# Kernel tuning notes

Hardware: AMD Instinct MI355X
Metric: run time of the kernel (lower is better)

## Reference

```python
import jax, jax.numpy as jnp
import numpy as np
import math

BS, H, L, D = 4, 8, 1024, 64
P = 513  # max_path_num + 1


def setup_inputs() -> dict:
    key = jax.random.key(0)
    ks = jax.random.split(key, 6)
    return {
        "query": jax.random.normal(ks[0], (BS, H, L, D), dtype=jnp.float32),
        "key": jax.random.normal(ks[1], (BS, H, L, D), dtype=jnp.float32),
        "value": jax.random.normal(ks[2], (BS, H, L, D), dtype=jnp.float32),
        "relation": jax.random.normal(ks[3], (BS, P, D), dtype=jnp.float32),
        "path_map": jax.random.randint(ks[4], (BS, L, L), 0, P, dtype=jnp.int32),
        "mask": jax.random.randint(ks[5], (BS, 1, L, L), 0, 2, dtype=jnp.int32),
    }


def reference(query, key, value, relation, path_map, mask):
    bs, h, Lc, d = query.shape
    p = relation.shape[1]
    # content score: bs,h,L,L
    score = jnp.einsum("bhik,bhjk->bhij", query, key)
    # relation score. Torch gathers with index of shape (bs,1,L,L) from a
    # (bs,h,L,P) tensor, which reads head 0 only and broadcasts over heads.
    score_r_h0 = jnp.einsum("bik,bpk->bip", query[:, 0], relation)  # bs,L,P
    gathered = jnp.take_along_axis(score_r_h0, path_map, axis=-1)   # bs,L,L
    score = score + gathered[:, None, :, :]
    scores = score / math.sqrt(d)
    scores = jnp.where(mask == 0, jnp.float32(-1e9), scores)
    p_attn = jax.nn.softmax(scores, axis=-1)  # bs,h,L,L
    attn_sum = jnp.einsum("bhij,bhjk->bhik", p_attn, value)
    # scatter-add attention probs into relation buckets: bs,h,L,P
    b_ix = jnp.arange(bs)[:, None, None, None]
    h_ix = jnp.arange(h)[None, :, None, None]
    i_ix = jnp.arange(Lc)[None, None, :, None]
    pm = jnp.broadcast_to(path_map[:, None, :, :], (bs, h, Lc, Lc))
    r_buckets = jnp.zeros((bs, h, Lc, p), dtype=p_attn.dtype).at[b_ix, h_ix, i_ix, pm].add(p_attn)
    r_attn_sum = jnp.einsum("bhip,bpk->bhik", r_buckets, relation)
    attn_sum = attn_sum + r_attn_sum
    return (attn_sum, p_attn)
```

## Files before the change

kernel.cpp:

```cpp
#include <hip/hip_runtime.h>


#define BSZ 4
#define NH 8
#define LSEQ 1024
#define DH 64
#define NP 513
#define TI 16
#define SRX 548
#define RTC 544

#define NQE (BSZ*NH*LSEQ*DH)
#define NRT (BSZ*DH*RTC)
#define NSR (BSZ*LSEQ*NP)
#define NGPW (2*BSZ*LSEQ*LSEQ)
#define OFF_QH 0
#define OFF_QL (NQE)
#define OFF_KH (2*NQE)
#define OFF_KL (3*NQE)
#define OFF_VT (4*NQE)
#define OFF_RT (5*NQE)
#define OFF_SR (5*NQE + NRT)
#define OFF_GP (5*NQE + NRT + NSR)
#define WS_NEED ((size_t)(OFF_GP + NGPW) * 2)

#define NB_SR 512
#define NB_QK 4096
#define NB_VT 512
#define NB_RT 544
#define NB_P1 (NB_SR + NB_QK + NB_VT + NB_RT)

typedef __attribute__((ext_vector_type(8))) short bf16x8;
typedef __attribute__((ext_vector_type(4))) float f32x4;
typedef __attribute__((ext_vector_type(4))) ushort u16x4;
typedef __attribute__((ext_vector_type(4))) uint u32x4;

__device__ __forceinline__ ushort f2bf(float x) {
    uint u = __float_as_uint(x);
    u += 0x7FFFu + ((u >> 16) & 1u);
    return (ushort)(u >> 16);
}
__device__ __forceinline__ float bf2f(ushort h) {
    return __uint_as_float(((uint)h) << 16);
}


__global__ __launch_bounds__(256) void prep1(
    const float* __restrict__ Q, const float* __restrict__ K,
    const float* __restrict__ V, const float* __restrict__ REL,
    ushort* __restrict__ ws)
{
    __shared__ float sT[64 * 65];
    const int bid = blockIdx.x;
    const int tid = threadIdx.x;

    if (bid < NB_SR) {
        const int b = bid >> 7;
        const int r = bid & 127;
        const int it = r >> 1, half = r & 1;
        const int i0 = it * TI;
        const int w = tid >> 6, l = tid & 63, lg = l >> 4, lm = l & 15;

        const float* Qb0 = Q + ((size_t)b * NH) * LSEQ * DH;
        const float* RELb = REL + (size_t)b * NP * DH;
        ushort* SRb = ws + OFF_SR + (size_t)b * LSEQ * NP;

        bf16x8 qh[2], ql[2];
        #pragma unroll
        for (int ks = 0; ks < 2; ++ks) {
            const float* qs = Qb0 + (size_t)(i0 + lm) * DH + ks * 32 + lg * 8;
            float4 v0 = *(const float4*)(qs);
            float4 v1 = *(const float4*)(qs + 4);
            float xs[8] = {v0.x, v0.y, v0.z, v0.w, v1.x, v1.y, v1.z, v1.w};
            #pragma unroll
            for (int e = 0; e < 8; ++e) {
                ushort hi = f2bf(xs[e]);
                qh[ks][e] = (short)hi;
                ql[ks][e] = (short)f2bf(xs[e] - bf2f(hi));
            }
        }

        int ctb = half ? 33 : 16;
        for (int ct = half * 16 + w; ct < ctb; ct += 4) {
            int p0 = ct * 16;
            int prow = p0 + lm; if (prow > 512) prow = 512;
            f32x4 a0 = {0.f, 0.f, 0.f, 0.f};
            #pragma unroll
            for (int ks = 0; ks < 2; ++ks) {
                const float* bsrc = RELb + (size_t)prow * DH + ks * 32 + lg * 8;
                float4 v0 = *(const float4*)(bsrc);
                float4 v1 = *(const float4*)(bsrc + 4);
                float xs[8] = {v0.x, v0.y, v0.z, v0.w, v1.x, v1.y, v1.z, v1.w};
                bf16x8 bh8, bl8;
                #pragma unroll
                for (int e = 0; e < 8; ++e) {
                    ushort hi = f2bf(xs[e]);
                    bh8[e] = (short)hi;
                    bl8[e] = (short)f2bf(xs[e] - bf2f(hi));
                }
                a0 = __builtin_amdgcn_mfma_f32_16x16x32_bf16(qh[ks], bh8, a0, 0, 0, 0);
                a0 = __builtin_amdgcn_mfma_f32_16x16x32_bf16(ql[ks], bh8, a0, 0, 0, 0);
                a0 = __builtin_amdgcn_mfma_f32_16x16x32_bf16(qh[ks], bl8, a0, 0, 0, 0);
            }
            if (p0 + lm < NP) {
                #pragma unroll
                for (int e = 0; e < 4; ++e)
                    SRb[(size_t)(i0 + 4 * lg + e) * NP + p0 + lm] = f2bf(a0[e]);
            }
        }
    } else if (bid < NB_SR + NB_QK) {
        const int n4 = NQE / 4;
        int i = (bid - NB_SR) * 256 + tid;
        int isK = i >= n4;
        int base = i - isK * n4;
        float4 v = ((const float4*)(isK ? K : Q))[base];
        float xs[4] = {v.x, v.y, v.z, v.w};
        u16x4 hh, ll;
        #pragma unroll
        for (int e = 0; e < 4; ++e) {
            ushort hi = f2bf(xs[e]);
            hh[e] = hi;
            ll[e] = f2bf(xs[e] - bf2f(hi));
        }
        *(u16x4*)(ws + (isK ? OFF_KH : OFF_QH) + (size_t)base * 4) = hh;
        *(u16x4*)(ws + (isK ? OFF_KL : OFF_QL) + (size_t)base * 4) = ll;
    } else if (bid < NB_SR + NB_QK + NB_VT) {
        const int vb = bid - (NB_SR + NB_QK);
        const int bh = vb >> 4;
        const int j0 = (vb & 15) * 64;
        const float* Vb = V + ((size_t)bh << 16);
        for (int i = tid; i < 1024; i += 256) {
            int jr = i >> 4, c4 = i & 15;
            float4 vv = *(const float4*)(Vb + (size_t)(j0 + jr) * DH + c4 * 4);
            float* dst = &sT[jr * 65 + c4 * 4];
            dst[0] = vv.x; dst[1] = vv.y; dst[2] = vv.z; dst[3] = vv.w;
        }
        __syncthreads();
        const int d = tid >> 2, jseg = tid & 3;
        ushort* dst = ws + OFF_VT + ((size_t)bh << 16) + (size_t)d * LSEQ + j0 + jseg * 16;
        #pragma unroll
        for (int g = 0; g < 4; ++g) {
            u16x4 o;
            #pragma unroll
            for (int e = 0; e < 4; ++e)
                o[e] = f2bf(sT[(jseg * 16 + g * 4 + e) * 65 + d]);
            *(u16x4*)(dst + g * 4) = o;
        }
    } else {
        int i = (bid - (NB_SR + NB_QK + NB_VT)) * 256 + tid;
        int b = i / (DH * RTC);
        int r = i - b * (DH * RTC);
        int d = r / RTC;
        int p = r - d * RTC;
        float x = (p < NP) ? REL[((size_t)b * NP + p) * DH + d] : 0.f;
        ws[OFF_RT + i] = f2bf(x);
    }
}


__global__ __launch_bounds__(256) void prep2(
    const int* __restrict__ PM, const int* __restrict__ MASK,
    ushort* __restrict__ ws)
{
    __shared__ ushort sSR[4 * 520];
    const int tid = threadIdx.x;
    const int bid = blockIdx.x;
    const int b = bid >> 8;
    const int row0 = (bid & 255) * 4;

    const ushort* SRb = ws + OFF_SR + (size_t)b * LSEQ * NP;
    uint* GPb = (uint*)(ws + OFF_GP) + (size_t)b * LSEQ * LSEQ;
    const int* PMb = PM + (size_t)b * LSEQ * LSEQ;
    const int* MKb = MASK + (size_t)b * LSEQ * LSEQ;

    for (int i = tid; i < 4 * 520; i += 256) {
        int row = i / 520, col = i - row * 520;
        if (col < NP) sSR[row * 520 + col] = SRb[(size_t)(row0 + row) * NP + col];
    }
    __syncthreads();

    #pragma unroll
    for (int r = 0; r < 4; ++r) {
        int idx4 = r * 256 + tid;
        int row = idx4 >> 8;
        int c0 = (idx4 & 255) * 4;
        size_t off = (size_t)(row0 + row) * LSEQ + c0;
        int4 pm4 = *(const int4*)(PMb + off);
        int4 mk4 = *(const int4*)(MKb + off);
        const ushort* srow = &sSR[row * 520];
        u32x4 o;
        o[0] = ((uint)(mk4.x ? srow[pm4.x] : 0xFF62u) << 16) | (uint)pm4.x;
        o[1] = ((uint)(mk4.y ? srow[pm4.y] : 0xFF62u) << 16) | (uint)pm4.y;
        o[2] = ((uint)(mk4.z ? srow[pm4.z] : 0xFF62u) << 16) | (uint)pm4.z;
        o[3] = ((uint)(mk4.w ? srow[pm4.w] : 0xFF62u) << 16) | (uint)pm4.w;
        *(u32x4*)(GPb + off) = o;
    }
}


__global__ __launch_bounds__(512, 4) void raa_qks(
    const ushort* __restrict__ ws, float* __restrict__ OUT_P)
{
    __shared__ float sRedM[16 * 9];
    __shared__ float sRedS[16 * 9];

    const int tid = threadIdx.x;
    const int w  = tid >> 6;
    const int l  = tid & 63;
    const int lg = l >> 4;
    const int lm = l & 15;

    const int bid = blockIdx.x;
    const int xcd = bid & 7;
    const int idx = bid >> 3;
    const int bh  = (xcd << 2) + (idx >> 6);
    const int it  = idx & 63;
    const int b   = bh >> 3;
    const int i0  = it * TI;

    const ushort* Qh = ws + OFF_QH + (size_t)bh * LSEQ * DH;
    const ushort* Ql = ws + OFF_QL + (size_t)bh * LSEQ * DH;
    const ushort* Kh = ws + OFF_KH + (size_t)bh * LSEQ * DH;
    const ushort* Kl = ws + OFF_KL + (size_t)bh * LSEQ * DH;
    const uint*   GPb = (const uint*)(ws + OFF_GP) + (size_t)b * LSEQ * LSEQ;

    float gf[32];
    #pragma unroll
    for (int t = 0; t < 8; ++t) {
        #pragma unroll
        for (int e = 0; e < 4; ++e) {
            int col = (8 * w + t) * 16 + lm;
            int row = 4 * lg + e;
            uint g = GPb[(size_t)(i0 + row) * LSEQ + col];
            gf[t * 4 + e] = bf2f((ushort)(g >> 16));
        }
    }

    bf16x8 qhh[2], qhl[2];
    #pragma unroll
    for (int ks = 0; ks < 2; ++ks) {
        size_t ao = (size_t)(i0 + lm) * DH + ks * 32 + lg * 8;
        qhh[ks] = *(const bf16x8*)(Qh + ao);
        qhl[ks] = *(const bf16x8*)(Ql + ao);
    }

    f32x4 acc[8];
    #pragma unroll
    for (int t = 0; t < 8; ++t) {
        size_t bo = (size_t)((8 * w + t) * 16 + lm) * DH + lg * 8;
        bf16x8 kh0 = *(const bf16x8*)(Kh + bo);
        bf16x8 kl0 = *(const bf16x8*)(Kl + bo);
        bf16x8 kh1 = *(const bf16x8*)(Kh + bo + 32);
        bf16x8 kl1 = *(const bf16x8*)(Kl + bo + 32);
        f32x4 a = {0.f, 0.f, 0.f, 0.f};
        a = __builtin_amdgcn_mfma_f32_16x16x32_bf16(qhh[0], kh0, a, 0, 0, 0);
        a = __builtin_amdgcn_mfma_f32_16x16x32_bf16(qhl[0], kh0, a, 0, 0, 0);
        a = __builtin_amdgcn_mfma_f32_16x16x32_bf16(qhh[0], kl0, a, 0, 0, 0);
        a = __builtin_amdgcn_mfma_f32_16x16x32_bf16(qhh[1], kh1, a, 0, 0, 0);
        a = __builtin_amdgcn_mfma_f32_16x16x32_bf16(qhl[1], kh1, a, 0, 0, 0);
        a = __builtin_amdgcn_mfma_f32_16x16x32_bf16(qhh[1], kl1, a, 0, 0, 0);
        acc[t] = a;
    }

    #pragma unroll
    for (int i = 0; i < 32; ++i) {
        int t = i >> 2, e = i & 3;
        float g = gf[i];
        acc[t][e] = (g < -1e30f) ? -1e9f : (acc[t][e] + g) * 0.125f;
    }

    float mw[4], c4v[4];
    #pragma unroll
    for (int e = 0; e < 4; ++e) {
        float m = acc[0][e];
        #pragma unroll
        for (int t = 1; t < 8; ++t) m = fmaxf(m, acc[t][e]);
        #pragma unroll
        for (int o = 8; o >= 1; o >>= 1) m = fmaxf(m, __shfl_xor(m, o));
        mw[e] = m;
        float s = 0.f;
        #pragma unroll
        for (int t = 0; t < 8; ++t) {
            float v = __expf(acc[t][e] - m);
            acc[t][e] = v;
            s += v;
        }
        #pragma unroll
        for (int o = 8; o >= 1; o >>= 1) s += __shfl_xor(s, o);
        if (lm == 0) {
            sRedM[(4 * lg + e) * 9 + w] = m;
            sRedS[(4 * lg + e) * 9 + w] = s;
        }
    }
    __syncthreads();
    #pragma unroll
    for (int e = 0; e < 4; ++e) {
        int row = 4 * lg + e;
        float mv = sRedM[row * 9 + (lm & 7)];
        float sv = sRedS[row * 9 + (lm & 7)];
        float m = mv;
        #pragma unroll
        for (int o = 4; o >= 1; o >>= 1) m = fmaxf(m, __shfl_xor(m, o));
        float sp = sv * __expf(mv - m);
        #pragma unroll
        for (int o = 4; o >= 1; o >>= 1) sp += __shfl_xor(sp, o);
        c4v[e] = __expf(mw[e] - m) / sp;
    }

    const size_t pbase = ((size_t)bh * LSEQ + i0) * LSEQ;
    #pragma unroll
    for (int t = 0; t < 8; ++t) {
        int col = (8 * w + t) * 16 + lm;
        #pragma unroll
        for (int e = 0; e < 4; ++e) {
            int row = 4 * lg + e;
            OUT_P[pbase + (size_t)row * LSEQ + col] = acc[t][e] * c4v[e];
        }
    }
}


__global__ __launch_bounds__(512, 4) void raa_pv(
    const ushort* __restrict__ ws, const float* __restrict__ P_in,
    float* __restrict__ OUT_A)
{
    __shared__ float X[TI * SRX];
    __shared__ float sAttn[TI * DH];

    const int tid = threadIdx.x;
    const int w  = tid >> 6;
    const int l  = tid & 63;
    const int lg = l >> 4;
    const int lm = l & 15;

    const int bid = blockIdx.x;
    const int xcd = bid & 7;
    const int idx = bid >> 3;
    const int bh  = (xcd << 2) + (idx >> 6);
    const int it  = idx & 63;
    const int b   = bh >> 3;
    const int i0  = it * TI;

    const ushort* Vt = ws + OFF_VT + (size_t)bh * DH * LSEQ;
    const ushort* Rt = ws + OFF_RT + (size_t)b * DH * RTC;
    const uint*   GPb = (const uint*)(ws + OFF_GP) + (size_t)b * LSEQ * LSEQ;
    const float*  Pb = P_in + ((size_t)bh * LSEQ + i0) * LSEQ;

    for (int z = tid; z < TI * SRX; z += 512) X[z] = 0.f;
    for (int z = tid; z < TI * DH; z += 512) sAttn[z] = 0.f;
    __syncthreads();

    {
        int row = 2 * w + (l >> 5);
        int l32 = l & 31;
        const float* prow = Pb + (size_t)row * LSEQ;
        const uint*  grow = GPb + (size_t)(i0 + row) * LSEQ;
        float* xrow = &X[row * SRX];
        #pragma unroll
        for (int itr = 0; itr < 8; ++itr) {
            int c0 = itr * 128 + l32 * 4;
            float4 p4 = *(const float4*)(prow + c0);
            u32x4 g4 = *(const u32x4*)(grow + c0);
            atomicAdd(&xrow[g4[0] & 0xFFFFu], p4.x);
            atomicAdd(&xrow[g4[1] & 0xFFFFu], p4.y);
            atomicAdd(&xrow[g4[2] & 0xFFFFu], p4.z);
            atomicAdd(&xrow[g4[3] & 0xFFFFu], p4.w);
        }
    }
    __syncthreads();

    const int d0 = (w & 3) * 16;
    f32x4 pa = {0.f, 0.f, 0.f, 0.f};
    if (w < 4) {
        #pragma unroll 4
        for (int ks = 0; ks < 32; ++ks) {
            int j0 = ks * 32;
            const float* ps = Pb + (size_t)lm * LSEQ + j0 + lg * 8;
            float4 a0 = *(const float4*)(ps);
            float4 a1 = *(const float4*)(ps + 4);
            bf16x8 a;
            a[0] = (short)f2bf(a0.x); a[1] = (short)f2bf(a0.y);
            a[2] = (short)f2bf(a0.z); a[3] = (short)f2bf(a0.w);
            a[4] = (short)f2bf(a1.x); a[5] = (short)f2bf(a1.y);
            a[6] = (short)f2bf(a1.z); a[7] = (short)f2bf(a1.w);
            bf16x8 bb = *(const bf16x8*)(Vt + (size_t)(d0 + lm) * LSEQ + j0 + lg * 8);
            pa = __builtin_amdgcn_mfma_f32_16x16x32_bf16(a, bb, pa, 0, 0, 0);
        }
    } else {
        #pragma unroll 4
        for (int ks = 0; ks < 17; ++ks) {
            int p0 = ks * 32;
            const float* xs = &X[lm * SRX + p0 + lg * 8];
            float4 a0 = *(const float4*)(xs);
            float4 a1 = *(const float4*)(xs + 4);
            bf16x8 a;
            a[0] = (short)f2bf(a0.x); a[1] = (short)f2bf(a0.y);
            a[2] = (short)f2bf(a0.z); a[3] = (short)f2bf(a0.w);
            a[4] = (short)f2bf(a1.x); a[5] = (short)f2bf(a1.y);
            a[6] = (short)f2bf(a1.z); a[7] = (short)f2bf(a1.w);
            bf16x8 bb = *(const bf16x8*)(Rt + (size_t)(d0 + lm) * RTC + p0 + lg * 8);
            pa = __builtin_amdgcn_mfma_f32_16x16x32_bf16(a, bb, pa, 0, 0, 0);
        }
    }
    #pragma unroll
    for (int e = 0; e < 4; ++e)
        atomicAdd(&sAttn[(4 * lg + e) * DH + d0 + lm], pa[e]);
    __syncthreads();

    {
        int row = tid >> 5;
        int c0 = (tid & 31) * 2;
        *(float2*)(OUT_A + ((size_t)bh * LSEQ + i0 + row) * DH + c0) =
            *(const float2*)&sAttn[row * DH + c0];
    }
}


__global__ __launch_bounds__(1024, 4) void raa_fallback(
    const float* __restrict__ Q, const float* __restrict__ K,
    const float* __restrict__ V, const float* __restrict__ REL,
    const int* __restrict__ PM, const int* __restrict__ MASK,
    float* __restrict__ OUT_A, float* __restrict__ OUT_P)
{
    __shared__ ushort sQh[TI * 64];
    __shared__ ushort sQl[TI * 64];
    __shared__ float  sR[TI * NP];
    __shared__ ushort sPb[TI * 1024];
    __shared__ float  sAttn[TI * 64];
    __shared__ float  sRed[16 * 17];
    __shared__ float  sFin[16];

    const int tid = threadIdx.x;
    const int w  = tid >> 6;
    const int l  = tid & 63;
    const int lg = l >> 4;
    const int lm = l & 15;

    const int it = blockIdx.x, h = blockIdx.y, b = blockIdx.z;
    const int i0 = it * TI;

    const float* Qb0  = Q + ((size_t)b * NH + 0) * LSEQ * DH;
    const float* Qbh  = Q + ((size_t)b * NH + h) * LSEQ * DH;
    const float* Kbh  = K + ((size_t)b * NH + h) * LSEQ * DH;
    const float* Vbh  = V + ((size_t)b * NH + h) * LSEQ * DH;
    const float* RELb = REL + (size_t)b * NP * DH;
    const int*   PMb  = PM  + (size_t)b * LSEQ * LSEQ;
    const int*   MKb  = MASK + (size_t)b * LSEQ * LSEQ;

    {
        int row = tid >> 6, kk = tid & 63;
        float x = Qb0[(size_t)(i0 + row) * DH + kk];
        ushort hi = f2bf(x);
        ushort lo = f2bf(x - bf2f(hi));
        int ad = row * 64 + (((kk >> 3) ^ (row & 7)) << 3) + (kk & 7);
        sQh[ad] = hi; sQl[ad] = lo;
        sAttn[tid] = 0.f;
    }
    __syncthreads();

    bf16x8 qh[2], ql[2];
    #pragma unroll
    for (int ks = 0; ks < 2; ++ks) {
        int ch = lg + 4 * ks;
        int ad = lm * 64 + ((ch ^ (lm & 7)) << 3);
        qh[ks] = *(const bf16x8*)&sQh[ad];
        ql[ks] = *(const bf16x8*)&sQl[ad];
    }
    __syncthreads();

    {
        int row = tid >> 6, kk = tid & 63;
        float x = Qbh[(size_t)(i0 + row) * DH + kk];
        ushort hi = f2bf(x);
        ushort lo = f2bf(x - bf2f(hi));
        int ad = row * 64 + (((kk >> 3) ^ (row & 7)) << 3) + (kk & 7);
        sQh[ad] = hi; sQl[ad] = lo;
    }

    for (int ct = w; ct < 33; ct += 16) {
        int p0 = ct * 16;
        int prow = p0 + lm; if (prow > 512) prow = 512;
        const float* bsrc = RELb + (size_t)prow * DH + 8 * lg;
        f32x4 acc = {0.f, 0.f, 0.f, 0.f};
        #pragma unroll
        for (int ks = 0; ks < 2; ++ks) {
            float4 v0 = *(const float4*)(bsrc + ks * 32);
            float4 v1 = *(const float4*)(bsrc + ks * 32 + 4);
            float xs[8] = {v0.x, v0.y, v0.z, v0.w, v1.x, v1.y, v1.z, v1.w};
            bf16x8 bh, bl;
            #pragma unroll
            for (int e = 0; e < 8; ++e) {
                ushort hi = f2bf(xs[e]);
                bh[e] = (short)hi;
                bl[e] = (short)f2bf(xs[e] - bf2f(hi));
            }
            acc = __builtin_amdgcn_mfma_f32_16x16x32_bf16(qh[ks], bh, acc, 0, 0, 0);
            acc = __builtin_amdgcn_mfma_f32_16x16x32_bf16(ql[ks], bh, acc, 0, 0, 0);
            acc = __builtin_amdgcn_mfma_f32_16x16x32_bf16(qh[ks], bl, acc, 0, 0, 0);
        }
        int pcol = p0 + lm;
        if (pcol < NP) {
            #pragma unroll
            for (int e = 0; e < 4; ++e)
                sR[(4 * lg + e) * NP + pcol] = acc[e];
        }
    }
    __syncthreads();

    #pragma unroll
    for (int ks = 0; ks < 2; ++ks) {
        int ch = lg + 4 * ks;
        int ad = lm * 64 + ((ch ^ (lm & 7)) << 3);
        qh[ks] = *(const bf16x8*)&sQh[ad];
        ql[ks] = *(const bf16x8*)&sQl[ad];
    }
    f32x4 acc[4];
    #pragma unroll
    for (int t = 0; t < 4; ++t) {
        int j = (4 * w + t) * 16 + lm;
        const float* bsrc = Kbh + (size_t)j * DH + 8 * lg;
        acc[t] = (f32x4){0.f, 0.f, 0.f, 0.f};
        #pragma unroll
        for (int ks = 0; ks < 2; ++ks) {
            float4 v0 = *(const float4*)(bsrc + ks * 32);
            float4 v1 = *(const float4*)(bsrc + ks * 32 + 4);
            float xs[8] = {v0.x, v0.y, v0.z, v0.w, v1.x, v1.y, v1.z, v1.w};
            bf16x8 bh, bl;
            #pragma unroll
            for (int e = 0; e < 8; ++e) {
                ushort hi = f2bf(xs[e]);
                bh[e] = (short)hi;
                bl[e] = (short)f2bf(xs[e] - bf2f(hi));
            }
            acc[t] = __builtin_amdgcn_mfma_f32_16x16x32_bf16(qh[ks], bh, acc[t], 0, 0, 0);
            acc[t] = __builtin_amdgcn_mfma_f32_16x16x32_bf16(ql[ks], bh, acc[t], 0, 0, 0);
            acc[t] = __builtin_amdgcn_mfma_f32_16x16x32_bf16(qh[ks], bl, acc[t], 0, 0, 0);
        }
    }

    #pragma unroll
    for (int t = 0; t < 4; ++t) {
        int col = (4 * w + t) * 16 + lm;
        #pragma unroll
        for (int e = 0; e < 4; ++e) {
            int row = 4 * lg + e;
            size_t off = (size_t)(i0 + row) * LSEQ + col;
            int pm = PMb[off];
            int mk = MKb[off];
            float g = sR[row * NP + pm];
            acc[t][e] = (mk == 0) ? -1e9f : (acc[t][e] + g) * 0.125f;
        }
    }
    __syncthreads();
    for (int idxx = tid; idxx < TI * NP; idxx += 1024) sR[idxx] = 0.f;
    __syncthreads();

    float Mr[4];
    #pragma unroll
    for (int e = 0; e < 4; ++e) {
        float m = fmaxf(fmaxf(acc[0][e], acc[1][e]), fmaxf(acc[2][e], acc[3][e]));
        #pragma unroll
        for (int o = 8; o >= 1; o >>= 1) m = fmaxf(m, __shfl_xor(m, o));
        Mr[e] = m;
    }
    if (lm == 0) {
        #pragma unroll
        for (int e = 0; e < 4; ++e) sRed[(4 * lg + e) * 17 + w] = Mr[e];
    }
    __syncthreads();
    if (w == 0 && l < 16) {
        float m = -INFINITY;
        for (int ww = 0; ww < 16; ++ww) m = fmaxf(m, sRed[l * 17 + ww]);
        sFin[l] = m;
    }
    __syncthreads();
    #pragma unroll
    for (int e = 0; e < 4; ++e) Mr[e] = sFin[4 * lg + e];

    float Sr[4];
    #pragma unroll
    for (int e = 0; e < 4; ++e) {
        float s = 0.f;
        #pragma unroll
        for (int t = 0; t < 4; ++t) {
            float v = __expf(acc[t][e] - Mr[e]);
            acc[t][e] = v;
            s += v;
        }
        #pragma unroll
        for (int o = 8; o >= 1; o >>= 1) s += __shfl_xor(s, o);
        Sr[e] = s;
    }
    if (lm == 0) {
        #pragma unroll
        for (int e = 0; e < 4; ++e) sRed[(4 * lg + e) * 17 + w] = Sr[e];
    }
    __syncthreads();
    if (w == 0 && l < 16) {
        float s = 0.f;
        for (int ww = 0; ww < 16; ++ww) s += sRed[l * 17 + ww];
        sFin[l] = s;
    }
    __syncthreads();

    float inv[4];
    #pragma unroll
    for (int e = 0; e < 4; ++e) inv[e] = 1.0f / sFin[4 * lg + e];

    const size_t pbase = (((size_t)b * NH + h) * LSEQ + i0) * LSEQ;
    #pragma unroll
    for (int t = 0; t < 4; ++t) {
        int col = (4 * w + t) * 16 + lm;
        #pragma unroll
        for (int e = 0; e < 4; ++e) {
            int row = 4 * lg + e;
            float p = acc[t][e] * inv[e];
            OUT_P[pbase + (size_t)row * LSEQ + col] = p;
            int ad = row * 1024 + (((col >> 3) ^ (row & 7)) << 3) + (col & 7);
            sPb[ad] = f2bf(p);
            int pm = PMb[(size_t)(i0 + row) * LSEQ + col];
            atomicAdd(&sR[row * NP + pm], p);
        }
    }
    __syncthreads();

    if (w < 8) {
        int ct = w >> 1, jh = w & 1;
        int d = ct * 16 + lm;
        f32x4 pa = {0.f, 0.f, 0.f, 0.f};
        for (int ks = 0; ks < 16; ++ks) {
            int j0 = jh * 512 + ks * 32;
            int ch = (j0 >> 3) + lg;
            bf16x8 a = *(const bf16x8*)&sPb[lm * 1024 + ((ch ^ (lm & 7)) << 3)];
            const float* vs = Vbh + (size_t)(j0 + 8 * lg) * DH + d;
            bf16x8 bb;
            #pragma unroll
            for (int e = 0; e < 8; ++e) bb[e] = (short)f2bf(vs[(size_t)e * DH]);
            pa = __builtin_amdgcn_mfma_f32_16x16x32_bf16(a, bb, pa, 0, 0, 0);
        }
        #pragma unroll
        for (int e = 0; e < 4; ++e)
            atomicAdd(&sAttn[(4 * lg + e) * 64 + d], pa[e]);
    } else {
        int ct = (w - 8) >> 1, ph = w & 1;
        int d = ct * 16 + lm;
        int nks = ph ? 9 : 8;
        f32x4 pa = {0.f, 0.f, 0.f, 0.f};
        for (int ks = 0; ks < nks; ++ks) {
            int p0 = ph * 256 + ks * 32 + 8 * lg;
            bf16x8 a, bb;
            #pragma unroll
            for (int e = 0; e < 8; ++e) {
                int pp = p0 + e;
                float av = (pp < NP) ? sR[lm * NP + pp] : 0.f;
                a[e] = (short)f2bf(av);
                int pc = (pp < NP) ? pp : (NP - 1);
                bb[e] = (short)f2bf(RELb[(size_t)pc * DH + d]);
            }
            pa = __builtin_amdgcn_mfma_f32_16x16x32_bf16(a, bb, pa, 0, 0, 0);
        }
        #pragma unroll
        for (int e = 0; e < 4; ++e)
            atomicAdd(&sAttn[(4 * lg + e) * 64 + d], pa[e]);
    }
    __syncthreads();

    {
        int row = tid >> 6, col = tid & 63;
        OUT_A[(((size_t)b * NH + h) * LSEQ + i0 + row) * DH + col] =
            sAttn[row * 64 + col];
    }
}

extern "C" void kernel_launch(void* const* d_in, const int* in_sizes, int n_in,
                              void* d_out, int out_size, void* d_ws, size_t ws_size,
                              hipStream_t stream) {
    const float* q    = (const float*)d_in[0];
    const float* k    = (const float*)d_in[1];
    const float* v    = (const float*)d_in[2];
    const float* rel  = (const float*)d_in[3];
    const int*   pm   = (const int*)d_in[4];
    const int*   mask = (const int*)d_in[5];
    float* out_a = (float*)d_out;
    float* out_p = (float*)d_out + (size_t)BSZ * NH * LSEQ * DH;

    if (ws_size >= WS_NEED && d_ws != nullptr) {
        ushort* ws = (ushort*)d_ws;
        prep1<<<NB_P1, 256, 0, stream>>>(q, k, v, rel, ws);
        prep2<<<1024, 256, 0, stream>>>(pm, mask, ws);
        raa_qks<<<2048, 512, 0, stream>>>((const ushort*)ws, out_p);
        raa_pv<<<2048, 512, 0, stream>>>((const ushort*)ws, out_p, out_a);
    } else {
        dim3 grid(LSEQ / TI, NH, BSZ);
        raa_fallback<<<grid, 1024, 0, stream>>>(q, k, v, rel, pm, mask, out_a, out_p);
    }
}
```

Measured before the change: 474.1 us.

## Stage P tile in swizzled LDS as bf16 and split PV work over 16 waves

raa_pv now launches 1024 threads per block. Each block loads its P tile and path indices once into registers, writes a bf16 copy of P into an XOR-swizzled LDS buffer, and performs the bucket scatter from the same registers. The P·V MMA then reads its A operand from LDS rather than re-reading fp32 P from global memory. The K dimension of both the PV and relation MMAs is split across twice as many waves, with partial results combined through LDS atomics. This adds 32KB of LDS per block and a larger block size, which may reduce occupancy.

```diff
diff --git a/kernel.cpp b/kernel.cpp
--- a/kernel.cpp
+++ b/kernel.cpp
@@ -320,12 +320,13 @@
 }
 
 
-__global__ __launch_bounds__(512, 4) void raa_pv(
+__global__ __launch_bounds__(1024, 8) void raa_pv(
     const ushort* __restrict__ ws, const float* __restrict__ P_in,
     float* __restrict__ OUT_A)
 {
-    __shared__ float X[TI * SRX];
-    __shared__ float sAttn[TI * DH];
+    __shared__ float  X[TI * SRX];
+    __shared__ ushort sPb[TI * 1024];
+    __shared__ float  sAttn[TI * DH];
 
     const int tid = threadIdx.x;
     const int w  = tid >> 6;
@@ -346,50 +347,62 @@
     const uint*   GPb = (const uint*)(ws + OFF_GP) + (size_t)b * LSEQ * LSEQ;
     const float*  Pb = P_in + ((size_t)bh * LSEQ + i0) * LSEQ;
 
-    for (int z = tid; z < TI * SRX; z += 512) X[z] = 0.f;
-    for (int z = tid; z < TI * DH; z += 512) sAttn[z] = 0.f;
-    __syncthreads();
-
-    {
-        int row = 2 * w + (l >> 5);
-        int l32 = l & 31;
-        const float* prow = Pb + (size_t)row * LSEQ;
-        const uint*  grow = GPb + (size_t)(i0 + row) * LSEQ;
-        float* xrow = &X[row * SRX];
-        #pragma unroll
-        for (int itr = 0; itr < 8; ++itr) {
-            int c0 = itr * 128 + l32 * 4;
-            float4 p4 = *(const float4*)(prow + c0);
-            u32x4 g4 = *(const u32x4*)(grow + c0);
-            atomicAdd(&xrow[g4[0] & 0xFFFFu], p4.x);
-            atomicAdd(&xrow[g4[1] & 0xFFFFu], p4.y);
-            atomicAdd(&xrow[g4[2] & 0xFFFFu], p4.z);
-            atomicAdd(&xrow[g4[3] & 0xFFFFu], p4.w);
-        }
+    float4 p4[4];
+    u32x4  g4[4];
+    #pragma unroll
+    for (int c = 0; c < 4; ++c) {
+        int flat = c * 4096 + tid * 4;
+        int r = flat >> 10, cc = flat & 1023;
+        p4[c] = *(const float4*)(Pb + (size_t)r * LSEQ + cc);
+        g4[c] = *(const u32x4*)(GPb + (size_t)(i0 + r) * LSEQ + cc);
+    }
+
+    #pragma unroll
+    for (int z = 0; z < 9; ++z) {
+        int zi = z * 1024 + tid;
+        if (zi < TI * SRX) X[zi] = 0.f;
+    }
+    sAttn[tid] = 0.f;
+    __syncthreads();
+
+    #pragma unroll
+    for (int c = 0; c < 4; ++c) {
+        int flat = c * 4096 + tid * 4;
+        int r = flat >> 10, cc = flat & 1023;
+        u16x4 pb;
+        pb[0] = f2bf(p4[c].x); pb[1] = f2bf(p4[c].y);
+        pb[2] = f2bf(p4[c].z); pb[3] = f2bf(p4[c].w);
+        int ch = cc >> 3;
+        int ad = r * 1024 + ((ch ^ (r & 7)) << 3) + (cc & 7);
+        *(u16x4*)&sPb[ad] = pb;
+        float* xrow = &X[r * SRX];
+        atomicAdd(&xrow[g4[c][0] & 0xFFFFu], p4[c].x);
+        atomicAdd(&xrow[g4[c][1] & 0xFFFFu], p4[c].y);
+        atomicAdd(&xrow[g4[c][2] & 0xFFFFu], p4[c].z);
+        atomicAdd(&xrow[g4[c][3] & 0xFFFFu], p4[c].w);
     }
     __syncthreads();
 
     const int d0 = (w & 3) * 16;
     f32x4 pa = {0.f, 0.f, 0.f, 0.f};
-    if (w < 4) {
-        #pragma unroll 4
-        for (int ks = 0; ks < 32; ++ks) {
-            int j0 = ks * 32;
-            const float* ps = Pb + (size_t)lm * LSEQ + j0 + lg * 8;
-            float4 a0 = *(const float4*)(ps);
-            float4 a1 = *(const float4*)(ps + 4);
-            bf16x8 a;
-            a[0] = (short)f2bf(a0.x); a[1] = (short)f2bf(a0.y);
-            a[2] = (short)f2bf(a0.z); a[3] = (short)f2bf(a0.w);
-            a[4] = (short)f2bf(a1.x); a[5] = (short)f2bf(a1.y);
-            a[6] = (short)f2bf(a1.z); a[7] = (short)f2bf(a1.w);
+    if (w < 8) {
+        const int jh = w >> 2;
+        #pragma unroll
+        for (int ks = 0; ks < 16; ++ks) {
+            int j0 = jh * 512 + ks * 32;
+            int ch = (j0 >> 3) + lg;
+            bf16x8 a = *(const bf16x8*)&sPb[lm * 1024 + ((ch ^ (lm & 7)) << 3)];
             bf16x8 bb = *(const bf16x8*)(Vt + (size_t)(d0 + lm) * LSEQ + j0 + lg * 8);
             pa = __builtin_amdgcn_mfma_f32_16x16x32_bf16(a, bb, pa, 0, 0, 0);
         }
     } else {
-        #pragma unroll 4
-        for (int ks = 0; ks < 17; ++ks) {
-            int p0 = ks * 32;
+        const int ph = (w - 8) >> 2;
+        const int nks = ph ? 8 : 9;
+        const int pb0 = ph ? 288 : 0;
+        #pragma unroll
+        for (int ks = 0; ks < 9; ++ks) {
+            if (ks >= nks) break;
+            int p0 = pb0 + ks * 32;
             const float* xs = &X[lm * SRX + p0 + lg * 8];
             float4 a0 = *(const float4*)(xs);
             float4 a1 = *(const float4*)(xs + 4);
@@ -407,12 +420,7 @@
         atomicAdd(&sAttn[(4 * lg + e) * DH + d0 + lm], pa[e]);
     __syncthreads();
 
-    {
-        int row = tid >> 5;
-        int c0 = (tid & 31) * 2;
-        *(float2*)(OUT_A + ((size_t)bh * LSEQ + i0 + row) * DH + c0) =
-            *(const float2*)&sAttn[row * DH + c0];
-    }
+    OUT_A[((size_t)bh * LSEQ + i0 + (tid >> 6)) * DH + (tid & 63)] = sAttn[tid];
 }
 
 
@@ -689,7 +697,7 @@
         prep1<<<NB_P1, 256, 0, stream>>>(q, k, v, rel, ws);
         prep2<<<1024, 256, 0, stream>>>(pm, mask, ws);
         raa_qks<<<2048, 512, 0, stream>>>((const ushort*)ws, out_p);
-        raa_pv<<<2048, 512, 0, stream>>>((const ushort*)ws, out_p, out_a);
+        raa_pv<<<2048, 1024, 0, stream>>>((const ushort*)ws, out_p, out_a);
     } else {
         dim3 grid(LSEQ / TI, NH, BSZ);
         raa_fallback<<<grid, 1024, 0, stream>>>(q, k, v, rel, pm, mask, out_a, out_p);
```

New measurement: 494.9 us. 4.4% more time.
